# Performance work log

Hardware: AMD Instinct MI355X
Metric: run time of the kernel (lower is better)

The kernel has to match this reference:

```python
import jax, jax.numpy as jnp
import numpy as np

N_NODES = 50000
IN_CH = 128
HID_CH = 128   # 2 * out_channels
OUT_CH = 64
N_EDGES = 800000


def setup_inputs() -> dict:
    key = jax.random.key(0)
    k1, k2, k3, k4 = jax.random.split(key, 4)
    x = jax.random.normal(k1, (N_NODES, IN_CH), dtype=jnp.float32)
    edge_index = jax.random.randint(k2, (2, N_EDGES), 0, N_NODES, dtype=jnp.int64)
    # Glorot-ish init for weights
    W1 = jax.random.normal(k3, (IN_CH, HID_CH), dtype=jnp.float32) * (1.0 / np.sqrt(IN_CH))
    b1 = jnp.zeros((HID_CH,), dtype=jnp.float32)
    W2 = jax.random.normal(k4, (HID_CH, OUT_CH), dtype=jnp.float32) * (1.0 / np.sqrt(HID_CH))
    b2 = jnp.zeros((OUT_CH,), dtype=jnp.float32)
    return {"x": x, "edge_index": edge_index, "W1": W1, "b1": b1, "W2": W2, "b2": b2}


def _gcn_norm(edge_index, num_nodes):
    """Add self-loops and compute symmetric normalization coeffs (PyG GCNConv default)."""
    loops = jnp.arange(num_nodes, dtype=edge_index.dtype)
    src = jnp.concatenate([edge_index[0], loops])  # [E + N]
    dst = jnp.concatenate([edge_index[1], loops])
    ones = jnp.ones_like(dst, dtype=jnp.float32)
    deg = jax.ops.segment_sum(ones, dst, num_segments=num_nodes)  # in-degree incl self-loop
    dinv = jnp.where(deg > 0, jax.lax.rsqrt(deg), 0.0)
    norm = dinv[src] * dinv[dst]  # [E + N]
    return src, dst, norm


def _gcn_conv(x, src, dst, norm, W, b, num_nodes):
    h = x @ W                                        # dense transform [N, d_out]
    msg = h[src] * norm[:, None]                     # gather + scale  [E+N, d_out]
    out = jax.ops.segment_sum(msg, dst, num_segments=num_nodes)  # scatter-add
    return out + b


def reference(x, edge_index, W1, b1, W2, b2):
    n = x.shape[0]
    src, dst, norm = _gcn_norm(edge_index, n)
    h = _gcn_conv(x, src, dst, norm, W1, b1, n)
    h = jax.nn.relu(h)
    out = _gcn_conv(h, src, dst, norm, W2, b2, n)
    return out
```

## Files before the change

### kernel.cpp

```cpp
#include <hip/hip_runtime.h>
#include <hip/hip_fp16.h>
#include <math.h>

#define IN_CH 128
#define CAP 64


__global__ __launch_bounds__(256, 4) void k_gemm_build(
    const float* __restrict__ x, const float* __restrict__ W1,
    __half* __restrict__ g1, int N,
    const int* __restrict__ src, const int* __restrict__ dst,
    int* __restrict__ deg, unsigned short* __restrict__ slot, int E, int GB) {
    constexpr int KC = 32;
    constexpr int AP = KC + 4;
    constexpr int NOUT = 128;
    constexpr int TCG = NOUT / 8;
    constexpr int BST = KC * 8 + 4;
    constexpr int TM = 4;
    __shared__ float As[64 * AP];
    __shared__ float Bs[TCG * BST];
    int tid = threadIdx.x;

    if ((int)blockIdx.x >= GB) {
        int base = ((int)blockIdx.x - GB) * 1024 + tid;
        int es[4], ed[4], er[4];
        bool ev[4];
#pragma unroll
        for (int k = 0; k < 4; ++k) {
            int e = base + k * 256;
            ev[k] = (e < E);
            ed[k] = ev[k] ? dst[e] : 0;
            es[k] = ev[k] ? src[e] : 0;
        }
#pragma unroll
        for (int k = 0; k < 4; ++k) er[k] = ev[k] ? atomicAdd(&deg[ed[k]], 1) : CAP;
#pragma unroll
        for (int k = 0; k < 4; ++k) {
            if (er[k] < CAP) slot[(size_t)ed[k] * CAP + er[k]] = (unsigned short)es[k];
        }
        return;
    }

    int row0 = (int)blockIdx.x * 64;
    int cg = tid % TCG;
    int rg = tid / TCG;
    int r0 = rg * TM;

    float acc[TM][8];
#pragma unroll
    for (int r = 0; r < TM; ++r)
#pragma unroll
        for (int c = 0; c < 8; ++c) acc[r][c] = 0.f;

    for (int kc0 = 0; kc0 < IN_CH; kc0 += KC) {
        if (kc0 > 0) __syncthreads();
        for (int idx = tid; idx < 64 * (KC / 4); idx += 256) {
            int r = idx >> 3;
            int c4 = (idx & 7) * 4;
            float4 v = make_float4(0.f, 0.f, 0.f, 0.f);
            if (row0 + r < N) v = *(const float4*)(x + (size_t)(row0 + r) * IN_CH + kc0 + c4);
            *(float4*)(As + r * AP + c4) = v;
        }
        for (int idx = tid; idx < KC * (NOUT / 4); idx += 256) {
            int kk = idx / (NOUT / 4);
            int col = (idx % (NOUT / 4)) * 4;
            int cgw = col >> 3;
            int j = col & 7;
            *(float4*)(Bs + cgw * BST + kk * 8 + j) = *(const float4*)(W1 + (size_t)(kc0 + kk) * NOUT + col);
        }
        __syncthreads();

        for (int k = 0; k < KC; k += 4) {
            float4 a4[TM];
#pragma unroll
            for (int r = 0; r < TM; ++r) a4[r] = *(const float4*)(As + (r0 + r) * AP + k);
#pragma unroll
            for (int kk = 0; kk < 4; ++kk) {
                float4 b0 = *(const float4*)(Bs + cg * BST + (k + kk) * 8);
                float4 b1 = *(const float4*)(Bs + cg * BST + (k + kk) * 8 + 4);
#pragma unroll
                for (int r = 0; r < TM; ++r) {
                    float a = (kk == 0) ? a4[r].x : (kk == 1) ? a4[r].y : (kk == 2) ? a4[r].z : a4[r].w;
                    acc[r][0] += a * b0.x;
                    acc[r][1] += a * b0.y;
                    acc[r][2] += a * b0.z;
                    acc[r][3] += a * b0.w;
                    acc[r][4] += a * b1.x;
                    acc[r][5] += a * b1.y;
                    acc[r][6] += a * b1.z;
                    acc[r][7] += a * b1.w;
                }
            }
        }
    }

#pragma unroll
    for (int r = 0; r < TM; ++r) {
        int row = row0 + r0 + r;
        if (row < N) {
            union { __half2 h[4]; uint4 u; } cv;
            cv.h[0] = __floats2half2_rn(acc[r][0], acc[r][1]);
            cv.h[1] = __floats2half2_rn(acc[r][2], acc[r][3]);
            cv.h[2] = __floats2half2_rn(acc[r][4], acc[r][5]);
            cv.h[3] = __floats2half2_rn(acc[r][6], acc[r][7]);
            *(uint4*)(g1 + (size_t)row * NOUT + cg * 8) = cv.u;
        }
    }
}

__global__ __launch_bounds__(256) void k_finish(
    const int* __restrict__ deg, float* __restrict__ dinv, __half* __restrict__ g1, int N) {
    int wave = threadIdx.x >> 6, lane = threadIdx.x & 63;
    int i = blockIdx.x * 4 + wave;
    if (i >= N) return;
    float d = rsqrtf((float)(deg[i] + 1));
    if (lane == 0) dinv[i] = d;
    __half2* gp = (__half2*)g1;
    float2 f = __half22float2(gp[(size_t)i * 64 + lane]);
    gp[(size_t)i * 64 + lane] = __floats2half2_rn(d * f.x, d * f.y);
}


__global__ __launch_bounds__(256, 4) void k_gemm64(
    const __half* __restrict__ A, const float* __restrict__ W,
    const float* __restrict__ dinv, __half* __restrict__ G, int M) {
    constexpr int KC = 32;
    constexpr int AP = KC + 4;
    constexpr int NOUT = 64;
    constexpr int TCG = NOUT / 8;
    constexpr int BST = KC * 8 + 4;
    constexpr int TM = 2;
    __shared__ float As[64 * AP];
    __shared__ float Bs[TCG * BST];
    int tid = threadIdx.x;
    int row0 = blockIdx.x * 64;
    int cg = tid % TCG;
    int rg = tid / TCG;
    int r0 = rg * TM;

    float acc[TM][8];
#pragma unroll
    for (int r = 0; r < TM; ++r)
#pragma unroll
        for (int c = 0; c < 8; ++c) acc[r][c] = 0.f;

    for (int kc0 = 0; kc0 < IN_CH; kc0 += KC) {
        if (kc0 > 0) __syncthreads();
        {
            int r = tid >> 2;
            int grp = tid & 3;
            float f[8];
            if (row0 + r < M) {
                uint4 raw = *(const uint4*)(A + (size_t)(row0 + r) * IN_CH + kc0 + grp * 8);
                const __half2* h2 = (const __half2*)&raw;
#pragma unroll
                for (int q = 0; q < 4; ++q) {
                    float2 fv = __half22float2(h2[q]);
                    f[2 * q] = fv.x;
                    f[2 * q + 1] = fv.y;
                }
            } else {
#pragma unroll
                for (int q = 0; q < 8; ++q) f[q] = 0.f;
            }
            *(float4*)(As + r * AP + grp * 8) = make_float4(f[0], f[1], f[2], f[3]);
            *(float4*)(As + r * AP + grp * 8 + 4) = make_float4(f[4], f[5], f[6], f[7]);
        }
        for (int idx = tid; idx < KC * (NOUT / 4); idx += 256) {
            int kk = idx / (NOUT / 4);
            int col = (idx % (NOUT / 4)) * 4;
            int cgw = col >> 3;
            int j = col & 7;
            *(float4*)(Bs + cgw * BST + kk * 8 + j) = *(const float4*)(W + (size_t)(kc0 + kk) * NOUT + col);
        }
        __syncthreads();

        for (int k = 0; k < KC; k += 4) {
            float4 a4[TM];
#pragma unroll
            for (int r = 0; r < TM; ++r) a4[r] = *(const float4*)(As + (r0 + r) * AP + k);
#pragma unroll
            for (int kk = 0; kk < 4; ++kk) {
                float4 b0 = *(const float4*)(Bs + cg * BST + (k + kk) * 8);
                float4 b1 = *(const float4*)(Bs + cg * BST + (k + kk) * 8 + 4);
#pragma unroll
                for (int r = 0; r < TM; ++r) {
                    float a = (kk == 0) ? a4[r].x : (kk == 1) ? a4[r].y : (kk == 2) ? a4[r].z : a4[r].w;
                    acc[r][0] += a * b0.x;
                    acc[r][1] += a * b0.y;
                    acc[r][2] += a * b0.z;
                    acc[r][3] += a * b0.w;
                    acc[r][4] += a * b1.x;
                    acc[r][5] += a * b1.y;
                    acc[r][6] += a * b1.z;
                    acc[r][7] += a * b1.w;
                }
            }
        }
    }

#pragma unroll
    for (int r = 0; r < TM; ++r) {
        int row = row0 + r0 + r;
        if (row < M) {
            float d = dinv[row];
            union { __half2 h[4]; uint4 u; } cv;
            cv.h[0] = __floats2half2_rn(d * acc[r][0], d * acc[r][1]);
            cv.h[1] = __floats2half2_rn(d * acc[r][2], d * acc[r][3]);
            cv.h[2] = __floats2half2_rn(d * acc[r][4], d * acc[r][5]);
            cv.h[3] = __floats2half2_rn(d * acc[r][6], d * acc[r][7]);
            *(uint4*)(G + (size_t)row * NOUT + cg * 8) = cv.u;
        }
    }
}


__global__ __launch_bounds__(256) void k_agg128(
    const __half* __restrict__ g, const float* __restrict__ dinv,
    const unsigned short* __restrict__ slot,
    const float* __restrict__ bias, __half* __restrict__ out, int N,
    const int* __restrict__ deg) {
    int wave = threadIdx.x >> 6, lane = threadIdx.x & 63;
    int i = blockIdx.x * 4 + wave;
    if (i >= N) return;
    const __half2* gp = (const __half2*)g;
    int m = min(deg[i], CAP);
    float dinv_i = dinv[i];
    float2 self = __half22float2(gp[(size_t)i * 64 + lane]);
    float2 acc = self;
    const unsigned short* sl = slot + (size_t)i * CAP;
    int r = 0;
    for (; r + 8 <= m; r += 8) {
        uint4 sraw = *(const uint4*)(sl + r);
        const unsigned short* sv = (const unsigned short*)&sraw;
        int s[8];
#pragma unroll
        for (int j = 0; j < 8; ++j) s[j] = sv[j];
        __half2 v[8];
#pragma unroll
        for (int j = 0; j < 8; ++j) v[j] = gp[(size_t)s[j] * 64 + lane];
#pragma unroll
        for (int j = 0; j < 8; ++j) {
            float2 f = __half22float2(v[j]);
            acc.x += f.x;
            acc.y += f.y;
        }
    }
    for (; r < m; ++r) {
        float2 f = __half22float2(gp[(size_t)sl[r] * 64 + lane]);
        acc.x += f.x;
        acc.y += f.y;
    }
    float2 b = ((const float2*)bias)[lane];
    float ox = fmaxf(dinv_i * acc.x + b.x, 0.f);
    float oy = fmaxf(dinv_i * acc.y + b.y, 0.f);
    ((__half2*)out)[(size_t)i * 64 + lane] = __floats2half2_rn(ox, oy);
}

__global__ __launch_bounds__(256) void k_agg64(
    const __half* __restrict__ g, const float* __restrict__ dinv,
    const unsigned short* __restrict__ slot,
    const float* __restrict__ bias, float* __restrict__ out, int N,
    const int* __restrict__ deg) {
    int wave = threadIdx.x >> 6, lane = threadIdx.x & 63;
    int half_id = lane >> 5;
    int ch = lane & 31;
    int i = (blockIdx.x * 4 + wave) * 2 + half_id;
    if (i >= N) return;
    const __half2* gp = (const __half2*)g;
    int m = min(deg[i], CAP);
    float dinv_i = dinv[i];
    float2 acc = __half22float2(gp[(size_t)i * 32 + ch]);
    const unsigned short* sl = slot + (size_t)i * CAP;
    int r = 0;
    for (; r + 8 <= m; r += 8) {
        uint4 sraw = *(const uint4*)(sl + r);
        const unsigned short* sv = (const unsigned short*)&sraw;
        int s[8];
#pragma unroll
        for (int j = 0; j < 8; ++j) s[j] = sv[j];
        __half2 v[8];
#pragma unroll
        for (int j = 0; j < 8; ++j) v[j] = gp[(size_t)s[j] * 32 + ch];
#pragma unroll
        for (int j = 0; j < 8; ++j) {
            float2 f = __half22float2(v[j]);
            acc.x += f.x;
            acc.y += f.y;
        }
    }
    for (; r < m; ++r) {
        float2 f = __half22float2(gp[(size_t)sl[r] * 32 + ch]);
        acc.x += f.x;
        acc.y += f.y;
    }
    float2 b = ((const float2*)bias)[ch];
    ((float2*)out)[(size_t)i * 32 + ch] =
        make_float2(dinv_i * acc.x + b.x, dinv_i * acc.y + b.y);
}


static inline size_t align256(size_t x) { return (x + 255) & ~(size_t)255; }

extern "C" void kernel_launch(void* const* d_in, const int* in_sizes, int n_in,
                              void* d_out, int out_size, void* d_ws, size_t ws_size,
                              hipStream_t stream) {
    const float* x = (const float*)d_in[0];
    const int* ei = (const int*)d_in[1];
    const float* W1 = (const float*)d_in[2];
    const float* b1 = (const float*)d_in[3];
    const float* W2 = (const float*)d_in[4];
    const float* b2 = (const float*)d_in[5];
    float* out = (float*)d_out;

    const int N = in_sizes[0] / IN_CH;
    const int E = in_sizes[1] / 2;
    const int* src = ei;
    const int* dst = ei + E;

    char* p = (char*)d_ws;
    int* deg = (int*)p;                 p += align256((size_t)N * 4);
    float* dinv = (float*)p;            p += align256((size_t)N * 4);
    unsigned short* slot = (unsigned short*)p;  p += align256((size_t)N * CAP * 2);
    __half* g1 = (__half*)p;            p += align256((size_t)N * 128 * 2);
    __half* a1 = (__half*)p;            p += align256((size_t)N * 128 * 2);
    __half* g2 = g1;

    const int GB = (N + 63) / 64;
    const int BB = (E + 1023) / 1024;

    hipMemsetAsync(deg, 0, (size_t)N * 4, stream);
    k_gemm_build<<<GB + BB, 256, 0, stream>>>(x, W1, g1, N, src, dst, deg, slot, E, GB);
    k_finish<<<(N + 3) / 4, 256, 0, stream>>>(deg, dinv, g1, N);
    k_agg128<<<(N + 3) / 4, 256, 0, stream>>>(g1, dinv, slot, b1, a1, N, deg);
    k_gemm64<<<GB, 256, 0, stream>>>(a1, W2, dinv, g2, N);
    k_agg64<<<(N + 7) / 8, 256, 0, stream>>>(g2, dinv, slot, b2, out, N, deg);
}
```

Measured before the change: 221.1 us.

## Partition edge-bucketing atomics by destination range per XCD for L2 locality

The edge-bucketing blocks now process 8192-edge chunks, with 8 blocks per chunk. Each block is tied to an XCD through blockIdx&7 and handles only the edges whose destination falls in that XCD's eighth of the node range. The goal is to keep the degree atomics and slot writes for a given node inside one XCD's L2 and avoid cross-die coherence traffic. In exchange, each block re-reads the dst array (8x total reads of dst) and adds a range check per edge. The dst loads are vectorized as int4. The scheme assumes round-robin dispatch of blocks to XCDs.

Result: no change. 217.7 us (-1.5%).

```diff
diff --git a/kernel.cpp b/kernel.cpp
--- a/kernel.cpp
+++ b/kernel.cpp
@@ -22,21 +22,42 @@
     int tid = threadIdx.x;
 
     if ((int)blockIdx.x >= GB) {
-        int base = ((int)blockIdx.x - GB) * 1024 + tid;
-        int es[4], ed[4], er[4];
-        bool ev[4];
-#pragma unroll
-        for (int k = 0; k < 4; ++k) {
-            int e = base + k * 256;
-            ev[k] = (e < E);
-            ed[k] = ev[k] ? dst[e] : 0;
-            es[k] = ev[k] ? src[e] : 0;
-        }
-#pragma unroll
-        for (int k = 0; k < 4; ++k) er[k] = ev[k] ? atomicAdd(&deg[ed[k]], 1) : CAP;
-#pragma unroll
-        for (int k = 0; k < 4; ++k) {
-            if (er[k] < CAP) slot[(size_t)ed[k] * CAP + er[k]] = (unsigned short)es[k];
+        int bb = (int)blockIdx.x - GB;
+        int xcd = (int)(blockIdx.x & 7);
+        int chunk = bb >> 3;
+        int cbase = chunk * 8192;
+        int ns = (N + 7) >> 3;
+        int lo = xcd * ns;
+        int hi = min(lo + ns, N);
+        int tid4 = tid * 4;
+#pragma unroll 2
+        for (int g = 0; g < 8; ++g) {
+            int e0 = cbase + g * 1024 + tid4;
+            if (e0 + 3 < E) {
+                int4 d4 = *(const int4*)(dst + e0);
+                int dd[4] = {d4.x, d4.y, d4.z, d4.w};
+#pragma unroll
+                for (int k = 0; k < 4; ++k) {
+                    int d = dd[k];
+                    if (d >= lo && d < hi) {
+                        int s = src[e0 + k];
+                        int r = atomicAdd(&deg[d], 1);
+                        if (r < CAP) slot[(size_t)d * CAP + r] = (unsigned short)s;
+                    }
+                }
+            } else {
+                for (int k = 0; k < 4; ++k) {
+                    int e = e0 + k;
+                    if (e < E) {
+                        int d = dst[e];
+                        if (d >= lo && d < hi) {
+                            int s = src[e];
+                            int r = atomicAdd(&deg[d], 1);
+                            if (r < CAP) slot[(size_t)d * CAP + r] = (unsigned short)s;
+                        }
+                    }
+                }
+            }
         }
         return;
     }
@@ -327,7 +348,8 @@
     __half* g2 = g1;
 
     const int GB = (N + 63) / 64;
-    const int BB = (E + 1023) / 1024;
+    const int CB = (E + 8191) / 8192;
+    const int BB = 8 * CB;
 
     hipMemsetAsync(deg, 0, (size_t)N * 4, stream);
     k_gemm_build<<<GB + BB, 256, 0, stream>>>(x, W1, g1, N, src, dst, deg, slot, E, GB);
```
